# Kernel tuning notes

Measured on AMD Instinct MI355X. Metric: run time of the kernel, lower is better.

## Reference

```python
import jax, jax.numpy as jnp
import numpy as np

NUM_ELEMENTS = 100
EMBED_DIM = 256
HIDDEN_DIM = 512
NUM_HEADS = 8
NUM_MASKS = 1
NUM_GAUSSIANS = 50
RBF_RADIUS = 12.0
N_NODES = 20000
N_EDGES = 400000


def setup_inputs() -> dict:
    key = jax.random.key(0)
    ks = jax.random.split(key, 10)
    anum = jax.random.randint(ks[0], (N_NODES,), 0, NUM_ELEMENTS)
    edge_index = jax.random.randint(ks[1], (2, N_EDGES), 0, N_NODES)
    edge_to_src = jax.random.randint(ks[2], (N_EDGES,), 0, N_EDGES)
    dist = jax.random.uniform(ks[3], (N_EDGES,), jnp.float32) * RBF_RADIUS
    # learned parameters (init scales follow reset_parameters)
    emb_table = jax.random.normal(ks[4], (NUM_ELEMENTS ** 2, EMBED_DIM), jnp.float32)
    s_gate = np.sqrt(3.0 / 2.50663)
    gate_W = jax.random.uniform(ks[5], (HIDDEN_DIM, NUM_GAUSSIANS), jnp.float32, -s_gate, s_gate)
    in_dim = EMBED_DIM + NUM_GAUSSIANS
    s_emb = np.sqrt(3.0 / EMBED_DIM)
    W_emb = jax.random.uniform(ks[6], (HIDDEN_DIM, EMBED_DIM), jnp.float32, -s_emb, s_emb)
    W_rbf = jax.random.uniform(ks[7], (HIDDEN_DIM, NUM_GAUSSIANS), jnp.float32, -s_gate, s_gate)
    W_in = jnp.concatenate([W_emb, W_rbf], axis=1)  # [H, emb+G]
    b_in = jnp.zeros((HIDDEN_DIM,), jnp.float32)
    s_out = np.sqrt(1.0 / HIDDEN_DIM)
    W_out = jax.random.uniform(ks[8], (NUM_HEADS * NUM_MASKS, HIDDEN_DIM), jnp.float32, -s_out, s_out)
    b_out = jnp.zeros((NUM_HEADS * NUM_MASKS,), jnp.float32)
    return {"anum": anum, "edge_index": edge_index, "edge_to_src": edge_to_src,
            "dist": dist, "emb_table": emb_table, "gate_W": gate_W,
            "W_in": W_in, "b_in": b_in, "W_out": W_out, "b_out": b_out}


def _gaussian_smearing(dist):
    offset = jnp.linspace(0.0, RBF_RADIUS, NUM_GAUSSIANS, dtype=dist.dtype)
    coeff = -0.5 / (offset[1] - offset[0]) ** 2
    d = dist[:, None] - offset[None, :]  # [E, G]
    return jnp.exp(coeff * d * d)


def reference(anum, edge_index, edge_to_src, dist, emb_table, gate_W, W_in, b_in, W_out, b_out):
    rbf = _gaussian_smearing(dist)                                  # [E, G]
    pair_idx = anum[edge_index[0]] + NUM_ELEMENTS * anum[edge_index[1]]  # [E]
    emb = emb_table[pair_idx]                                       # [E, D]
    x = jnp.concatenate([emb[edge_to_src], rbf], axis=-1)           # [E, D+G]
    gate = rbf @ gate_W.T                                           # [E, H]
    h = jax.nn.silu(x @ W_in.T + b_in) * gate                       # gated ResMLP hidden
    att_bias = h @ W_out.T + b_out                                  # [E, heads*masks]
    att_bias = att_bias.reshape(dist.shape[0], NUM_HEADS, NUM_MASKS)
    return jnp.transpose(att_bias, (2, 1, 0))                       # [masks, heads, E]
```

## Files before the change

### kernel.cpp

```cpp
#include <hip/hip_runtime.h>
#include <hip/hip_bf16.h>

typedef unsigned short u16;
typedef unsigned int   uint;
typedef __attribute__((ext_vector_type(8))) short bf16x8;
typedef __attribute__((ext_vector_type(4))) float f32x4;

constexpr int NELEM = 100;
constexpr int EMBED = 256;
constexpr int HID   = 512;
constexpr int KX    = 306;
constexpr int G     = 50;
constexpr int M     = 64;
constexpr int THREADS = 512;

constexpr int WB_ELEMS = 32 * 10 * 64 * 8;
constexpr int GB_ELEMS = 32 * 2 * 64 * 8;
constexpr int OB_ELEMS = 16 * 64 * 8;
constexpr int WEIGHT_ELEMS = WB_ELEMS + GB_ELEMS + OB_ELEMS;
constexpr int NPREP = WEIGHT_ELEMS / THREADS;

__device__ __forceinline__ u16 f2bf(float x) {
    uint u = __float_as_uint(x);
    u = (u + 0x7fffu + ((u >> 16) & 1u)) >> 16;
    return (u16)u;
}
__device__ __forceinline__ uint pk2(float a, float b) {
    __hip_bfloat162 h = __float22bfloat162_rn(make_float2(a, b));
    return *reinterpret_cast<uint*>(&h);
}
__device__ __forceinline__ float bflo(uint u) { return __uint_as_float(u << 16); }
__device__ __forceinline__ float bfhi(uint u) { return __uint_as_float(u & 0xffff0000u); }
__device__ __forceinline__ float silu(float p) {
    return p * __builtin_amdgcn_rcpf(1.f + __expf(-p));
}
__device__ __forceinline__ f32x4 mfma16(bf16x8 a, bf16x8 b, f32x4 c) {
    return __builtin_amdgcn_mfma_f32_16x16x32_bf16(a, b, c, 0, 0, 0);
}

__global__ __launch_bounds__(THREADS)
void prep_hist_kernel(const float* __restrict__ W_in,
                      const float* __restrict__ gate_W,
                      const float* __restrict__ W_out,
                      const float* __restrict__ b_in,
                      const int* __restrict__ anum,
                      const int* __restrict__ edge_index,
                      const int* __restrict__ edge_to_src,
                      u16* __restrict__ Wb,
                      u16* __restrict__ Gb,
                      u16* __restrict__ Ob,
                      u16* __restrict__ pairids,
                      int* __restrict__ bins,
                      int E) {
    const int bid = blockIdx.x;
    const int t   = threadIdx.x;

    if (bid < NPREP) {
        int idx = bid * THREADS + t;
        if (idx < WB_ELEMS) {
            int j = idx & 7, lane = (idx >> 3) & 63, kn = idx >> 9;
            int ks = kn % 10, nt = kn / 10;
            int h = nt * 16 + (lane & 15);
            int k = ks * 32 + (lane >> 4) * 8 + j;
            float v = (k < KX) ? W_in[h * KX + k] : ((k == KX) ? b_in[h] : 0.f);
            Wb[idx] = f2bf(v);
        } else if (idx < WB_ELEMS + GB_ELEMS) {
            int i2 = idx - WB_ELEMS;
            int j = i2 & 7, lane = (i2 >> 3) & 63, kn = i2 >> 9;
            int ks = kn & 1, nt = kn >> 1;
            int h = nt * 16 + (lane & 15);
            int g = ks * 32 + (lane >> 4) * 8 + j;
            Gb[i2] = f2bf((g < G) ? gate_W[h * G + g] : 0.f);
        } else {
            int i2 = idx - WB_ELEMS - GB_ELEMS;
            int j = i2 & 7, lane = (i2 >> 3) & 63, s = i2 >> 9;
            int m = lane & 15, q = lane >> 4;
            int hid = s * 32 + (j >> 2) * 16 + q * 4 + (j & 3);
            Ob[i2] = f2bf((m < 8) ? W_out[m * HID + hid] : 0.f);
        }
        return;
    }
    int i = (bid - NPREP) * THREADS + t;
    if (i < E) {
        int src  = edge_to_src[i];
        int pair = anum[edge_index[src]] + NELEM * anum[edge_index[E + src]];
        pairids[i] = (u16)pair;
        atomicAdd(&bins[pair], 1);
    }
}

__global__ __launch_bounds__(THREADS)
void scan_kernel(int* __restrict__ bins, int npair) {
    __shared__ int lds[THREADS];
    const int t = threadIdx.x;
    const int chunk = (npair + THREADS - 1) / THREADS;
    const int lo = t * chunk;
    const int hi = min(lo + chunk, npair);
    int s = 0;
    for (int i = lo; i < hi; ++i) s += bins[i];
    lds[t] = s;
    __syncthreads();
    for (int off = 1; off < THREADS; off <<= 1) {
        int add = (t >= off) ? lds[t - off] : 0;
        __syncthreads();
        lds[t] += add;
        __syncthreads();
    }
    int excl = lds[t] - s;
    for (int i = lo; i < hi; ++i) {
        int c = bins[i];
        bins[i] = excl;
        excl += c;
    }
}

__global__ __launch_bounds__(THREADS)
void scatter_hpre_kernel(const float* __restrict__ table,
                         const u16* __restrict__ Wb,
                         const u16* __restrict__ pairids,
                         int* __restrict__ bins,
                         int* __restrict__ perm,
                         u16* __restrict__ spair,
                         float* __restrict__ hpreF,
                         u16*   __restrict__ hpreH,
                         int E, int npair, int nsc, int f32h) {
    __shared__ __align__(16) u16 af[8 * 4 * 64 * 8];
    const int bid = blockIdx.x;
    const int t   = threadIdx.x;

    if (bid < nsc) {
        int i = bid * THREADS + t;
        if (i < E) {
            int p   = pairids[i];
            int pos = atomicAdd(&bins[p], 1);
            perm[pos]  = i;
            spair[pos] = (u16)p;
        }
        return;
    }

    const int pb = bid - nsc;
    const int p0 = pb * M;
    const int wave = t >> 6, lane = t & 63;
    const int col = lane & 15, quad = lane >> 4;

    #pragma unroll
    for (int mt = 0; mt < 4; ++mt) {
        int p = p0 + mt * 16 + col;
        uint4 w = {0u, 0u, 0u, 0u};
        if (p < npair) {
            const float* s = table + (size_t)p * EMBED + wave * 32 + quad * 8;
            float4 v0 = ((const float4*)s)[0], v1 = ((const float4*)s)[1];
            w.x = pk2(v0.x, v0.y); w.y = pk2(v0.z, v0.w);
            w.z = pk2(v1.x, v1.y); w.w = pk2(v1.z, v1.w);
        }
        *(uint4*)&af[((wave * 4 + mt) * 64 + lane) * 8] = w;
    }
    __syncthreads();

    const f32x4 z4 = {0.f, 0.f, 0.f, 0.f};
    #pragma unroll
    for (int nh = 0; nh < 2; ++nh) {
        f32x4 acc[2][4];
        #pragma unroll
        for (int ntl = 0; ntl < 2; ++ntl)
            #pragma unroll
            for (int mt = 0; mt < 4; ++mt) acc[ntl][mt] = z4;
        #pragma unroll 2
        for (int ks = 0; ks < 8; ++ks) {
            bf16x8 a[4];
            #pragma unroll
            for (int mt = 0; mt < 4; ++mt)
                a[mt] = *(const bf16x8*)&af[((ks * 4 + mt) * 64 + lane) * 8];
            #pragma unroll
            for (int ntl = 0; ntl < 2; ++ntl) {
                int ntg = wave * 4 + nh * 2 + ntl;
                bf16x8 wf = *(const bf16x8*)&Wb[((ntg * 10 + ks) * 64 + lane) * 8];
                #pragma unroll
                for (int mt = 0; mt < 4; ++mt)
                    acc[ntl][mt] = mfma16(wf, a[mt], acc[ntl][mt]);
            }
        }
        #pragma unroll
        for (int ntl = 0; ntl < 2; ++ntl)
            #pragma unroll
            for (int mt = 0; mt < 4; ++mt) {
                int p = p0 + mt * 16 + col;
                if (p < npair) {
                    int hb = (wave * 4 + nh * 2 + ntl) * 16 + quad * 4;
                    if (f32h) {
                        *(f32x4*)(hpreF + (size_t)p * HID + hb) = acc[ntl][mt];
                    } else {
                        uint2 o;
                        o.x = pk2(acc[ntl][mt][0], acc[ntl][mt][1]);
                        o.y = pk2(acc[ntl][mt][2], acc[ntl][mt][3]);
                        *(uint2*)(hpreH + (size_t)p * HID + hb) = o;
                    }
                }
            }
    }
}

template <bool F32H>
__global__ __launch_bounds__(THREADS, 4)
void pair_embed_srt(const int* __restrict__ perm,
                    const u16* __restrict__ spair,
                    const float* __restrict__ dist,
                    const float* __restrict__ hpreF,
                    const u16*   __restrict__ hpreH,
                    const float* __restrict__ b_out,
                    const u16* __restrict__ Wb,
                    const u16* __restrict__ Gb,
                    const u16* __restrict__ Ob,
                    float* __restrict__ out,
                    int E) {
    __shared__ __align__(16) u16 smem[16384];
    __shared__ int   rowbase[M];
    __shared__ float dste[M];
    __shared__ int   oidx[M];
    u16*   afrag = smem;
    float* redf  = (float*)smem;

    const int t  = threadIdx.x;
    const int e0 = blockIdx.x * M;
    const int wave = t >> 6, lane = t & 63;
    const int col = lane & 15, quad = lane >> 4;

    if (t < M) {
        int slot = e0 + t;
        int pair = 0, orig = 0; float d = 0.f;
        if (slot < E) {
            orig = perm[slot];
            pair = spair[slot];
            d    = dist[orig];
        }
        rowbase[t] = pair * HID;
        dste[t]    = d;
        oidx[t]    = orig;
    }
    __syncthreads();

    int rbm[4];
    #pragma unroll
    for (int mt = 0; mt < 4; ++mt) rbm[mt] = rowbase[mt * 16 + col];

    f32x4 hp[2][4];
    uint2 hph[2][4];
    #pragma unroll
    for (int mt = 0; mt < 4; ++mt) {
        int base = rbm[mt] + (wave * 4) * 16 + quad * 4;
        if (F32H) {
            const float* p = hpreF + base;
            hp[0][mt] = *(const f32x4*)p;
            hp[1][mt] = *(const f32x4*)(p + 16);
        } else {
            const u16* p = hpreH + base;
            hph[0][mt] = *(const uint2*)p;
            hph[1][mt] = *(const uint2*)(p + 16);
        }
    }

    {
        const float sp    = 12.0f / 49.0f;
        const float coeff = -0.5f / (sp * sp);
        int ks = wave & 1, mtr = wave >> 1;
        float d  = dste[mtr * 16 + col];
        int   g0 = ks * 32 + quad * 8;
        float f[8];
        #pragma unroll
        for (int j = 0; j < 8; ++j) {
            int g = g0 + j;
            float dd = d - sp * (float)g;
            f[j] = (g < G) ? __expf(coeff * dd * dd) : ((g == G) ? 1.f : 0.f);
        }
        uint4 w;
        w.x = pk2(f[0], f[1]); w.y = pk2(f[2], f[3]);
        w.z = pk2(f[4], f[5]); w.w = pk2(f[6], f[7]);
        *(uint4*)&afrag[((ks * 4 + mtr) * 64 + lane) * 8] = w;
    }
    __syncthreads();

    const f32x4 z4 = {0.f, 0.f, 0.f, 0.f};
    f32x4 oacc[4] = {z4, z4, z4, z4};

    #pragma unroll
    for (int nh = 0; nh < 2; ++nh) {
        if (nh == 1) {
            #pragma unroll
            for (int mt = 0; mt < 4; ++mt) {
                int base = rbm[mt] + (wave * 4 + 2) * 16 + quad * 4;
                if (F32H) {
                    const float* p = hpreF + base;
                    hp[0][mt] = *(const f32x4*)p;
                    hp[1][mt] = *(const f32x4*)(p + 16);
                } else {
                    const u16* p = hpreH + base;
                    hph[0][mt] = *(const uint2*)p;
                    hph[1][mt] = *(const uint2*)(p + 16);
                }
            }
        }
        f32x4 acc[2][4], gacc[2][4];
        #pragma unroll
        for (int ntl = 0; ntl < 2; ++ntl)
            #pragma unroll
            for (int mt = 0; mt < 4; ++mt) {
                gacc[ntl][mt] = z4;
                if (F32H) {
                    acc[ntl][mt] = hp[ntl][mt];
                } else {
                    uint2 v = hph[ntl][mt];
                    f32x4 a = {bflo(v.x), bfhi(v.x), bflo(v.y), bfhi(v.y)};
                    acc[ntl][mt] = a;
                }
            }

        const u16* gb = &Gb[((wave * 4 + nh * 2) * 2 * 64 + lane) * 8];
        const u16* wb = &Wb[(((wave * 4 + nh * 2) * 10 + 8) * 64 + lane) * 8];
        #pragma unroll
        for (int ks = 0; ks < 2; ++ks) {
            bf16x8 a[4];
            #pragma unroll
            for (int mt = 0; mt < 4; ++mt)
                a[mt] = *(const bf16x8*)&afrag[((ks * 4 + mt) * 64 + lane) * 8];
            bf16x8 g0f = *(const bf16x8*)&gb[ks * 512];
            bf16x8 w0f = *(const bf16x8*)&wb[ks * 512];
            bf16x8 g1f = *(const bf16x8*)&gb[1024 + ks * 512];
            bf16x8 w1f = *(const bf16x8*)&wb[5120 + ks * 512];
            #pragma unroll
            for (int mt = 0; mt < 4; ++mt) gacc[0][mt] = mfma16(g0f, a[mt], gacc[0][mt]);
            #pragma unroll
            for (int mt = 0; mt < 4; ++mt) acc[0][mt]  = mfma16(w0f, a[mt], acc[0][mt]);
            #pragma unroll
            for (int mt = 0; mt < 4; ++mt) gacc[1][mt] = mfma16(g1f, a[mt], gacc[1][mt]);
            #pragma unroll
            for (int mt = 0; mt < 4; ++mt) acc[1][mt]  = mfma16(w1f, a[mt], acc[1][mt]);
        }

        bf16x8 obf = *(const bf16x8*)&Ob[(((wave << 1) | nh) * 64 + lane) * 8];
        #pragma unroll
        for (int mt = 0; mt < 4; ++mt) {
            uint4 hq;
            hq.x = pk2(silu(acc[0][mt][0]) * gacc[0][mt][0],
                       silu(acc[0][mt][1]) * gacc[0][mt][1]);
            hq.y = pk2(silu(acc[0][mt][2]) * gacc[0][mt][2],
                       silu(acc[0][mt][3]) * gacc[0][mt][3]);
            hq.z = pk2(silu(acc[1][mt][0]) * gacc[1][mt][0],
                       silu(acc[1][mt][1]) * gacc[1][mt][1]);
            hq.w = pk2(silu(acc[1][mt][2]) * gacc[1][mt][2],
                       silu(acc[1][mt][3]) * gacc[1][mt][3]);
            oacc[mt] = mfma16(obf, *(bf16x8*)&hq, oacc[mt]);
        }
    }
    __syncthreads();

    #pragma unroll
    for (int mt = 0; mt < 4; ++mt)
        *(f32x4*)&redf[((wave * 4 + mt) * 64 + lane) * 4] = oacc[mt];
    __syncthreads();

    {
        int head = t >> 6, el = t & 63;
        int mt = el >> 4, c = el & 15;
        int l  = (head >> 2) * 16 + c;
        int r  = head & 3;
        float s = 0.f;
        #pragma unroll
        for (int w = 0; w < 8; ++w)
            s += redf[((w * 4 + mt) * 64 + l) * 4 + r];
        int slot = e0 + el;
        if (slot < E) out[head * E + oidx[el]] = s + b_out[head];
    }
}

template <bool F32H>
__global__ __launch_bounds__(THREADS, 4)
void pair_embed_pre(const int* __restrict__ anum,
                    const int* __restrict__ edge_index,
                    const int* __restrict__ edge_to_src,
                    const float* __restrict__ dist,
                    const float* __restrict__ hpreF,
                    const u16*   __restrict__ hpreH,
                    const float* __restrict__ b_out,
                    const u16* __restrict__ Wb,
                    const u16* __restrict__ Gb,
                    const u16* __restrict__ Ob,
                    float* __restrict__ out,
                    int E) {
    __shared__ __align__(16) u16 smem[16384];
    __shared__ int   rowbase[M];
    __shared__ float dste[M];
    u16*   afrag = smem;
    float* redf  = (float*)smem;

    const int t  = threadIdx.x;
    const int e0 = blockIdx.x * M;
    const int wave = t >> 6, lane = t & 63;
    const int col = lane & 15, quad = lane >> 4;

    if (t < M) {
        int eg = e0 + t;
        int pair = 0; float d = 0.f;
        if (eg < E) {
            int src = edge_to_src[eg];
            pair = anum[edge_index[src]] + NELEM * anum[edge_index[E + src]];
            d = dist[eg];
        }
        rowbase[t] = pair * HID;
        dste[t]    = d;
    }
    __syncthreads();

    int rbm[4];
    #pragma unroll
    for (int mt = 0; mt < 4; ++mt) rbm[mt] = rowbase[mt * 16 + col];

    f32x4 hp[2][4];
    uint2 hph[2][4];
    #pragma unroll
    for (int mt = 0; mt < 4; ++mt) {
        int base = rbm[mt] + (wave * 4) * 16 + quad * 4;
        if (F32H) {
            const float* p = hpreF + base;
            hp[0][mt] = *(const f32x4*)p;
            hp[1][mt] = *(const f32x4*)(p + 16);
        } else {
            const u16* p = hpreH + base;
            hph[0][mt] = *(const uint2*)p;
            hph[1][mt] = *(const uint2*)(p + 16);
        }
    }

    {
        const float sp    = 12.0f / 49.0f;
        const float coeff = -0.5f / (sp * sp);
        int ks = wave & 1, mtr = wave >> 1;
        float d  = dste[mtr * 16 + col];
        int   g0 = ks * 32 + quad * 8;
        float f[8];
        #pragma unroll
        for (int j = 0; j < 8; ++j) {
            int g = g0 + j;
            float dd = d - sp * (float)g;
            f[j] = (g < G) ? __expf(coeff * dd * dd) : ((g == G) ? 1.f : 0.f);
        }
        uint4 w;
        w.x = pk2(f[0], f[1]); w.y = pk2(f[2], f[3]);
        w.z = pk2(f[4], f[5]); w.w = pk2(f[6], f[7]);
        *(uint4*)&afrag[((ks * 4 + mtr) * 64 + lane) * 8] = w;
    }
    __syncthreads();

    const f32x4 z4 = {0.f, 0.f, 0.f, 0.f};
    f32x4 oacc[4] = {z4, z4, z4, z4};

    #pragma unroll
    for (int nh = 0; nh < 2; ++nh) {
        if (nh == 1) {
            #pragma unroll
            for (int mt = 0; mt < 4; ++mt) {
                int base = rbm[mt] + (wave * 4 + 2) * 16 + quad * 4;
                if (F32H) {
                    const float* p = hpreF + base;
                    hp[0][mt] = *(const f32x4*)p;
                    hp[1][mt] = *(const f32x4*)(p + 16);
                } else {
                    const u16* p = hpreH + base;
                    hph[0][mt] = *(const uint2*)p;
                    hph[1][mt] = *(const uint2*)(p + 16);
                }
            }
        }
        f32x4 acc[2][4], gacc[2][4];
        #pragma unroll
        for (int ntl = 0; ntl < 2; ++ntl)
            #pragma unroll
            for (int mt = 0; mt < 4; ++mt) {
                gacc[ntl][mt] = z4;
                if (F32H) {
                    acc[ntl][mt] = hp[ntl][mt];
                } else {
                    uint2 v = hph[ntl][mt];
                    f32x4 a = {bflo(v.x), bfhi(v.x), bflo(v.y), bfhi(v.y)};
                    acc[ntl][mt] = a;
                }
            }

        const u16* gb = &Gb[((wave * 4 + nh * 2) * 2 * 64 + lane) * 8];
        const u16* wb = &Wb[(((wave * 4 + nh * 2) * 10 + 8) * 64 + lane) * 8];
        #pragma unroll
        for (int ks = 0; ks < 2; ++ks) {
            bf16x8 a[4];
            #pragma unroll
            for (int mt = 0; mt < 4; ++mt)
                a[mt] = *(const bf16x8*)&afrag[((ks * 4 + mt) * 64 + lane) * 8];
            bf16x8 g0f = *(const bf16x8*)&gb[ks * 512];
            bf16x8 w0f = *(const bf16x8*)&wb[ks * 512];
            bf16x8 g1f = *(const bf16x8*)&gb[1024 + ks * 512];
            bf16x8 w1f = *(const bf16x8*)&wb[5120 + ks * 512];
            #pragma unroll
            for (int mt = 0; mt < 4; ++mt) gacc[0][mt] = mfma16(g0f, a[mt], gacc[0][mt]);
            #pragma unroll
            for (int mt = 0; mt < 4; ++mt) acc[0][mt]  = mfma16(w0f, a[mt], acc[0][mt]);
            #pragma unroll
            for (int mt = 0; mt < 4; ++mt) gacc[1][mt] = mfma16(g1f, a[mt], gacc[1][mt]);
            #pragma unroll
            for (int mt = 0; mt < 4; ++mt) acc[1][mt]  = mfma16(w1f, a[mt], acc[1][mt]);
        }

        bf16x8 obf = *(const bf16x8*)&Ob[(((wave << 1) | nh) * 64 + lane) * 8];
        #pragma unroll
        for (int mt = 0; mt < 4; ++mt) {
            uint4 hq;
            hq.x = pk2(silu(acc[0][mt][0]) * gacc[0][mt][0],
                       silu(acc[0][mt][1]) * gacc[0][mt][1]);
            hq.y = pk2(silu(acc[0][mt][2]) * gacc[0][mt][2],
                       silu(acc[0][mt][3]) * gacc[0][mt][3]);
            hq.z = pk2(silu(acc[1][mt][0]) * gacc[1][mt][0],
                       silu(acc[1][mt][1]) * gacc[1][mt][1]);
            hq.w = pk2(silu(acc[1][mt][2]) * gacc[1][mt][2],
                       silu(acc[1][mt][3]) * gacc[1][mt][3]);
            oacc[mt] = mfma16(obf, *(bf16x8*)&hq, oacc[mt]);
        }
    }
    __syncthreads();

    #pragma unroll
    for (int mt = 0; mt < 4; ++mt)
        *(f32x4*)&redf[((wave * 4 + mt) * 64 + lane) * 4] = oacc[mt];
    __syncthreads();

    {
        int head = t >> 6, el = t & 63;
        int mt = el >> 4, c = el & 15;
        int l  = (head >> 2) * 16 + c;
        int r  = head & 3;
        float s = 0.f;
        #pragma unroll
        for (int w = 0; w < 8; ++w)
            s += redf[((w * 4 + mt) * 64 + l) * 4 + r];
        int eg = e0 + el;
        if (eg < E) out[head * E + eg] = s + b_out[head];
    }
}

extern "C" void kernel_launch(void* const* d_in, const int* in_sizes, int n_in,
                              void* d_out, int out_size, void* d_ws, size_t ws_size,
                              hipStream_t stream) {
    const int*   anum        = (const int*)d_in[0];
    const int*   edge_index  = (const int*)d_in[1];
    const int*   edge_to_src = (const int*)d_in[2];
    const float* dist        = (const float*)d_in[3];
    const float* emb_table   = (const float*)d_in[4];
    const float* gate_W      = (const float*)d_in[5];
    const float* W_in        = (const float*)d_in[6];
    const float* b_in        = (const float*)d_in[7];
    const float* W_out       = (const float*)d_in[8];
    const float* b_out       = (const float*)d_in[9];
    const int E     = in_sizes[3];
    const int TBL   = in_sizes[4];
    const int NPAIR = TBL / EMBED;

    u16* Wb = (u16*)d_ws;
    u16* Gb = Wb + WB_ELEMS;
    u16* Ob = Gb + GB_ELEMS;
    const size_t WSW  = (size_t)WEIGHT_ELEMS * 2;
    const size_t hb32 = (size_t)NPAIR * HID * 4;
    const size_t hb16 = (size_t)NPAIR * HID * 2;
    const size_t sortx = (size_t)E * 8 + (size_t)NPAIR * 4;

    int mode;
    if      (ws_size >= WSW + hb32 + sortx) mode = 4;
    else if (ws_size >= WSW + hb16 + sortx) mode = 3;
    else if (ws_size >= WSW + hb32)         mode = 2;
    else                                    mode = 1;

    const size_t hb = (mode == 4 || mode == 2) ? hb32 : hb16;
    char*  hbase   = (char*)d_ws + WSW;
    float* hpreF   = (float*)hbase;
    u16*   hpreH   = (u16*)hbase;
    char*  q       = hbase + hb;
    int*   perm    = (int*)q;
    u16*   pairids = (u16*)(q + (size_t)E * 4);
    u16*   spair   = (u16*)(q + (size_t)E * 6);
    int*   bins    = (int*)(q + (size_t)E * 8);

    const int nhist   = (E + THREADS - 1) / THREADS;
    const int npb     = (NPAIR + M - 1) / M;
    const int nblocks = (E + M - 1) / M;
    const int f32h    = (mode == 4 || mode == 2) ? 1 : 0;

    if (mode >= 3) {
        hipMemsetAsync(bins, 0, (size_t)NPAIR * 4, stream);
        prep_hist_kernel<<<NPREP + nhist, THREADS, 0, stream>>>(
            W_in, gate_W, W_out, b_in, anum, edge_index, edge_to_src,
            Wb, Gb, Ob, pairids, bins, E);
        scan_kernel<<<1, THREADS, 0, stream>>>(bins, NPAIR);
        scatter_hpre_kernel<<<nhist + npb, THREADS, 0, stream>>>(
            emb_table, Wb, pairids, bins, perm, spair, hpreF, hpreH,
            E, NPAIR, nhist, f32h);
        if (mode == 4) {
            pair_embed_srt<true><<<nblocks, THREADS, 0, stream>>>(
                perm, spair, dist, hpreF, hpreH, b_out, Wb, Gb, Ob, (float*)d_out, E);
        } else {
            pair_embed_srt<false><<<nblocks, THREADS, 0, stream>>>(
                perm, spair, dist, hpreF, hpreH, b_out, Wb, Gb, Ob, (float*)d_out, E);
        }
    } else {
        prep_hist_kernel<<<NPREP, THREADS, 0, stream>>>(
            W_in, gate_W, W_out, b_in, anum, edge_index, edge_to_src,
            Wb, Gb, Ob, pairids, bins, E);
        scatter_hpre_kernel<<<npb, THREADS, 0, stream>>>(
            emb_table, Wb, pairids, bins, perm, spair, hpreF, hpreH,
            E, NPAIR, 0, f32h);
        if (mode == 2) {
            pair_embed_pre<true><<<nblocks, THREADS, 0, stream>>>(
                anum, edge_index, edge_to_src, dist, hpreF, hpreH,
                b_out, Wb, Gb, Ob, (float*)d_out, E);
        } else {
            pair_embed_pre<false><<<nblocks, THREADS, 0, stream>>>(
                anum, edge_index, edge_to_src, dist, hpreF, hpreH,
                b_out, Wb, Gb, Ob, (float*)d_out, E);
        }
    }
}
```

Baseline: 293.2 us.

## Restructure sort pipeline: fuse hist with hpre GEMM, pack sorted edges, drop bf16 modes

```diff
diff --git a/kernel.cpp b/kernel.cpp
--- a/kernel.cpp
+++ b/kernel.cpp
@@ -18,7 +18,6 @@
 constexpr int GB_ELEMS = 32 * 2 * 64 * 8;
 constexpr int OB_ELEMS = 16 * 64 * 8;
 constexpr int WEIGHT_ELEMS = WB_ELEMS + GB_ELEMS + OB_ELEMS;
-constexpr int NPREP = WEIGHT_ELEMS / THREADS;
 
 __device__ __forceinline__ u16 f2bf(float x) {
     uint u = __float_as_uint(x);
@@ -29,8 +28,6 @@
     __hip_bfloat162 h = __float22bfloat162_rn(make_float2(a, b));
     return *reinterpret_cast<uint*>(&h);
 }
-__device__ __forceinline__ float bflo(uint u) { return __uint_as_float(u << 16); }
-__device__ __forceinline__ float bfhi(uint u) { return __uint_as_float(u & 0xffff0000u); }
 __device__ __forceinline__ float silu(float p) {
     return p * __builtin_amdgcn_rcpf(1.f + __expf(-p));
 }
@@ -39,24 +36,20 @@
 }
 
 __global__ __launch_bounds__(THREADS)
-void prep_hist_kernel(const float* __restrict__ W_in,
-                      const float* __restrict__ gate_W,
-                      const float* __restrict__ W_out,
-                      const float* __restrict__ b_in,
-                      const int* __restrict__ anum,
-                      const int* __restrict__ edge_index,
-                      const int* __restrict__ edge_to_src,
-                      u16* __restrict__ Wb,
-                      u16* __restrict__ Gb,
-                      u16* __restrict__ Ob,
-                      u16* __restrict__ pairids,
-                      int* __restrict__ bins,
-                      int E) {
-    const int bid = blockIdx.x;
-    const int t   = threadIdx.x;
-
-    if (bid < NPREP) {
-        int idx = bid * THREADS + t;
+void init_kernel(const float* __restrict__ W_in,
+                 const float* __restrict__ gate_W,
+                 const float* __restrict__ W_out,
+                 const float* __restrict__ b_in,
+                 u16* __restrict__ Wb,
+                 u16* __restrict__ Gb,
+                 u16* __restrict__ Ob,
+                 int* __restrict__ bins,
+                 int npair, int do_sort) {
+    const int gtid = blockIdx.x * THREADS + threadIdx.x;
+    const int gsz  = gridDim.x * THREADS;
+    if (do_sort)
+        for (int i = gtid; i < npair; i += gsz) bins[i] = 0;
+    for (int idx = gtid; idx < WEIGHT_ELEMS; idx += gsz) {
         if (idx < WB_ELEMS) {
             int j = idx & 7, lane = (idx >> 3) & 63, kn = idx >> 9;
             int ks = kn % 10, nt = kn / 10;
@@ -78,14 +71,96 @@
             int hid = s * 32 + (j >> 2) * 16 + q * 4 + (j & 3);
             Ob[i2] = f2bf((m < 8) ? W_out[m * HID + hid] : 0.f);
         }
+    }
+}
+
+__global__ __launch_bounds__(THREADS)
+void hist_hpre_kernel(const int* __restrict__ anum,
+                      const int* __restrict__ edge_index,
+                      const int* __restrict__ edge_to_src,
+                      const float* __restrict__ table,
+                      const u16* __restrict__ Wb,
+                      u16* __restrict__ pairids,
+                      int* __restrict__ bins,
+                      float* __restrict__ hpreF,
+                      int E, int npair, int nh4) {
+    __shared__ __align__(16) u16 af[8 * 4 * 64 * 8];
+    const int bid = blockIdx.x;
+    const int t   = threadIdx.x;
+
+    if (bid < nh4) {
+        const int base = bid * (THREADS * 4) + t;
+        int idxv[4], srcv[4], n0[4], n1[4];
+        #pragma unroll
+        for (int k = 0; k < 4; ++k) idxv[k] = base + k * THREADS;
+        #pragma unroll
+        for (int k = 0; k < 4; ++k)
+            if (idxv[k] < E) srcv[k] = edge_to_src[idxv[k]];
+        #pragma unroll
+        for (int k = 0; k < 4; ++k)
+            if (idxv[k] < E) { n0[k] = edge_index[srcv[k]]; n1[k] = edge_index[E + srcv[k]]; }
+        #pragma unroll
+        for (int k = 0; k < 4; ++k)
+            if (idxv[k] < E) {
+                int pair = anum[n0[k]] + NELEM * anum[n1[k]];
+                pairids[idxv[k]] = (u16)pair;
+                atomicAdd(&bins[pair], 1);
+            }
         return;
     }
-    int i = (bid - NPREP) * THREADS + t;
-    if (i < E) {
-        int src  = edge_to_src[i];
-        int pair = anum[edge_index[src]] + NELEM * anum[edge_index[E + src]];
-        pairids[i] = (u16)pair;
-        atomicAdd(&bins[pair], 1);
+
+    const int pb = bid - nh4;
+    const int p0 = pb * M;
+    const int wave = t >> 6, lane = t & 63;
+    const int col = lane & 15, quad = lane >> 4;
+
+    #pragma unroll
+    for (int mt = 0; mt < 4; ++mt) {
+        int p = p0 + mt * 16 + col;
+        uint4 w = {0u, 0u, 0u, 0u};
+        if (p < npair) {
+            const float* s = table + (size_t)p * EMBED + wave * 32 + quad * 8;
+            float4 v0 = ((const float4*)s)[0], v1 = ((const float4*)s)[1];
+            w.x = pk2(v0.x, v0.y); w.y = pk2(v0.z, v0.w);
+            w.z = pk2(v1.x, v1.y); w.w = pk2(v1.z, v1.w);
+        }
+        *(uint4*)&af[((wave * 4 + mt) * 64 + lane) * 8] = w;
+    }
+    __syncthreads();
+
+    const f32x4 z4 = {0.f, 0.f, 0.f, 0.f};
+    #pragma unroll
+    for (int nh = 0; nh < 2; ++nh) {
+        f32x4 acc[2][4];
+        #pragma unroll
+        for (int ntl = 0; ntl < 2; ++ntl)
+            #pragma unroll
+            for (int mt = 0; mt < 4; ++mt) acc[ntl][mt] = z4;
+        #pragma unroll 2
+        for (int ks = 0; ks < 8; ++ks) {
+            bf16x8 a[4];
+            #pragma unroll
+            for (int mt = 0; mt < 4; ++mt)
+                a[mt] = *(const bf16x8*)&af[((ks * 4 + mt) * 64 + lane) * 8];
+            #pragma unroll
+            for (int ntl = 0; ntl < 2; ++ntl) {
+                int ntg = wave * 4 + nh * 2 + ntl;
+                bf16x8 wf = *(const bf16x8*)&Wb[((ntg * 10 + ks) * 64 + lane) * 8];
+                #pragma unroll
+                for (int mt = 0; mt < 4; ++mt)
+                    acc[ntl][mt] = mfma16(wf, a[mt], acc[ntl][mt]);
+            }
+        }
+        #pragma unroll
+        for (int ntl = 0; ntl < 2; ++ntl)
+            #pragma unroll
+            for (int mt = 0; mt < 4; ++mt) {
+                int p = p0 + mt * 16 + col;
+                if (p < npair) {
+                    int hb = (wave * 4 + nh * 2 + ntl) * 16 + quad * 4;
+                    *(f32x4*)(hpreF + (size_t)p * HID + hb) = acc[ntl][mt];
+                }
+            }
     }
 }
 
@@ -115,99 +190,29 @@
 }
 
 __global__ __launch_bounds__(THREADS)
-void scatter_hpre_kernel(const float* __restrict__ table,
-                         const u16* __restrict__ Wb,
-                         const u16* __restrict__ pairids,
-                         int* __restrict__ bins,
-                         int* __restrict__ perm,
-                         u16* __restrict__ spair,
-                         float* __restrict__ hpreF,
-                         u16*   __restrict__ hpreH,
-                         int E, int npair, int nsc, int f32h) {
-    __shared__ __align__(16) u16 af[8 * 4 * 64 * 8];
-    const int bid = blockIdx.x;
-    const int t   = threadIdx.x;
-
-    if (bid < nsc) {
-        int i = bid * THREADS + t;
-        if (i < E) {
-            int p   = pairids[i];
-            int pos = atomicAdd(&bins[p], 1);
-            perm[pos]  = i;
-            spair[pos] = (u16)p;
-        }
-        return;
-    }
-
-    const int pb = bid - nsc;
-    const int p0 = pb * M;
-    const int wave = t >> 6, lane = t & 63;
-    const int col = lane & 15, quad = lane >> 4;
-
-    #pragma unroll
-    for (int mt = 0; mt < 4; ++mt) {
-        int p = p0 + mt * 16 + col;
-        uint4 w = {0u, 0u, 0u, 0u};
-        if (p < npair) {
-            const float* s = table + (size_t)p * EMBED + wave * 32 + quad * 8;
-            float4 v0 = ((const float4*)s)[0], v1 = ((const float4*)s)[1];
-            w.x = pk2(v0.x, v0.y); w.y = pk2(v0.z, v0.w);
-            w.z = pk2(v1.x, v1.y); w.w = pk2(v1.z, v1.w);
-        }
-        *(uint4*)&af[((wave * 4 + mt) * 64 + lane) * 8] = w;
-    }
-    __syncthreads();
-
-    const f32x4 z4 = {0.f, 0.f, 0.f, 0.f};
-    #pragma unroll
-    for (int nh = 0; nh < 2; ++nh) {
-        f32x4 acc[2][4];
-        #pragma unroll
-        for (int ntl = 0; ntl < 2; ++ntl)
-            #pragma unroll
-            for (int mt = 0; mt < 4; ++mt) acc[ntl][mt] = z4;
-        #pragma unroll 2
-        for (int ks = 0; ks < 8; ++ks) {
-            bf16x8 a[4];
-            #pragma unroll
-            for (int mt = 0; mt < 4; ++mt)
-                a[mt] = *(const bf16x8*)&af[((ks * 4 + mt) * 64 + lane) * 8];
-            #pragma unroll
-            for (int ntl = 0; ntl < 2; ++ntl) {
-                int ntg = wave * 4 + nh * 2 + ntl;
-                bf16x8 wf = *(const bf16x8*)&Wb[((ntg * 10 + ks) * 64 + lane) * 8];
-                #pragma unroll
-                for (int mt = 0; mt < 4; ++mt)
-                    acc[ntl][mt] = mfma16(wf, a[mt], acc[ntl][mt]);
-            }
-        }
-        #pragma unroll
-        for (int ntl = 0; ntl < 2; ++ntl)
-            #pragma unroll
-            for (int mt = 0; mt < 4; ++mt) {
-                int p = p0 + mt * 16 + col;
-                if (p < npair) {
-                    int hb = (wave * 4 + nh * 2 + ntl) * 16 + quad * 4;
-                    if (f32h) {
-                        *(f32x4*)(hpreF + (size_t)p * HID + hb) = acc[ntl][mt];
-                    } else {
-                        uint2 o;
-                        o.x = pk2(acc[ntl][mt][0], acc[ntl][mt][1]);
-                        o.y = pk2(acc[ntl][mt][2], acc[ntl][mt][3]);
-                        *(uint2*)(hpreH + (size_t)p * HID + hb) = o;
-                    }
-                }
-            }
-    }
-}
-
-template <bool F32H>
-__global__ __launch_bounds__(THREADS, 4)
-void pair_embed_srt(const int* __restrict__ perm,
-                    const u16* __restrict__ spair,
+void scatter_kernel(const u16* __restrict__ pairids,
+                    int* __restrict__ bins,
+                    uint2* __restrict__ sedge,
+                    int E) {
+    const int base = blockIdx.x * (THREADS * 4) + threadIdx.x;
+    int idxv[4], pv[4];
+    #pragma unroll
+    for (int k = 0; k < 4; ++k) idxv[k] = base + k * THREADS;
+    #pragma unroll
+    for (int k = 0; k < 4; ++k)
+        if (idxv[k] < E) pv[k] = pairids[idxv[k]];
+    #pragma unroll
+    for (int k = 0; k < 4; ++k)
+        if (idxv[k] < E) {
+            int pos = atomicAdd(&bins[pv[k]], 1);
+            sedge[pos] = make_uint2((uint)idxv[k], (uint)pv[k]);
+        }
+}
+
+__global__ __launch_bounds__(THREADS, 3)
+void pair_embed_srt(const uint2* __restrict__ sedge,
                     const float* __restrict__ dist,
                     const float* __restrict__ hpreF,
-                    const u16*   __restrict__ hpreH,
                     const float* __restrict__ b_out,
                     const u16* __restrict__ Wb,
                     const u16* __restrict__ Gb,
@@ -228,15 +233,12 @@
 
     if (t < M) {
         int slot = e0 + t;
-        int pair = 0, orig = 0; float d = 0.f;
-        if (slot < E) {
-            orig = perm[slot];
-            pair = spair[slot];
-            d    = dist[orig];
-        }
-        rowbase[t] = pair * HID;
+        uint2 se = make_uint2(0u, 0u);
+        float d = 0.f;
+        if (slot < E) { se = sedge[slot]; d = dist[se.x]; }
+        rowbase[t] = (int)se.y * HID;
         dste[t]    = d;
-        oidx[t]    = orig;
+        oidx[t]    = (int)se.x;
     }
     __syncthreads();
 
@@ -244,20 +246,12 @@
     #pragma unroll
     for (int mt = 0; mt < 4; ++mt) rbm[mt] = rowbase[mt * 16 + col];
 
-    f32x4 hp[2][4];
-    uint2 hph[2][4];
+    f32x4 hp0[2][4];
     #pragma unroll
     for (int mt = 0; mt < 4; ++mt) {
-        int base = rbm[mt] + (wave * 4) * 16 + quad * 4;
-        if (F32H) {
-            const float* p = hpreF + base;
-            hp[0][mt] = *(const f32x4*)p;
-            hp[1][mt] = *(const f32x4*)(p + 16);
-        } else {
-            const u16* p = hpreH + base;
-            hph[0][mt] = *(const uint2*)p;
-            hph[1][mt] = *(const uint2*)(p + 16);
-        }
+        const float* p = hpreF + rbm[mt] + wave * 64 + quad * 4;
+        hp0[0][mt] = *(const f32x4*)p;
+        hp0[1][mt] = *(const f32x4*)(p + 16);
     }
 
     {
@@ -280,39 +274,26 @@
     }
     __syncthreads();
 
+    f32x4 hp1[2][4];
+    #pragma unroll
+    for (int mt = 0; mt < 4; ++mt) {
+        const float* p = hpreF + rbm[mt] + wave * 64 + 32 + quad * 4;
+        hp1[0][mt] = *(const f32x4*)p;
+        hp1[1][mt] = *(const f32x4*)(p + 16);
+    }
+
     const f32x4 z4 = {0.f, 0.f, 0.f, 0.f};
     f32x4 oacc[4] = {z4, z4, z4, z4};
 
     #pragma unroll
     for (int nh = 0; nh < 2; ++nh) {
-        if (nh == 1) {
-            #pragma unroll
-            for (int mt = 0; mt < 4; ++mt) {
-                int base = rbm[mt] + (wave * 4 + 2) * 16 + quad * 4;
-                if (F32H) {
-                    const float* p = hpreF + base;
-                    hp[0][mt] = *(const f32x4*)p;
-                    hp[1][mt] = *(const f32x4*)(p + 16);
-                } else {
-                    const u16* p = hpreH + base;
-                    hph[0][mt] = *(const uint2*)p;
-                    hph[1][mt] = *(const uint2*)(p + 16);
-                }
-            }
-        }
         f32x4 acc[2][4], gacc[2][4];
         #pragma unroll
         for (int ntl = 0; ntl < 2; ++ntl)
             #pragma unroll
             for (int mt = 0; mt < 4; ++mt) {
                 gacc[ntl][mt] = z4;
-                if (F32H) {
-                    acc[ntl][mt] = hp[ntl][mt];
-                } else {
-                    uint2 v = hph[ntl][mt];
-                    f32x4 a = {bflo(v.x), bfhi(v.x), bflo(v.y), bfhi(v.y)};
-                    acc[ntl][mt] = a;
-                }
+                acc[ntl][mt]  = nh ? hp1[ntl][mt] : hp0[ntl][mt];
             }
 
         const u16* gb = &Gb[((wave * 4 + nh * 2) * 2 * 64 + lane) * 8];
@@ -373,20 +354,18 @@
     }
 }
 
-template <bool F32H>
 __global__ __launch_bounds__(THREADS, 4)
-void pair_embed_pre(const int* __restrict__ anum,
-                    const int* __restrict__ edge_index,
-                    const int* __restrict__ edge_to_src,
-                    const float* __restrict__ dist,
-                    const float* __restrict__ hpreF,
-                    const u16*   __restrict__ hpreH,
-                    const float* __restrict__ b_out,
-                    const u16* __restrict__ Wb,
-                    const u16* __restrict__ Gb,
-                    const u16* __restrict__ Ob,
-                    float* __restrict__ out,
-                    int E) {
+void pair_embed_unsrt(const int* __restrict__ anum,
+                      const int* __restrict__ edge_index,
+                      const int* __restrict__ edge_to_src,
+                      const float* __restrict__ dist,
+                      const float* __restrict__ hpreF,
+                      const float* __restrict__ b_out,
+                      const u16* __restrict__ Wb,
+                      const u16* __restrict__ Gb,
+                      const u16* __restrict__ Ob,
+                      float* __restrict__ out,
+                      int E) {
     __shared__ __align__(16) u16 smem[16384];
     __shared__ int   rowbase[M];
     __shared__ float dste[M];
@@ -416,19 +395,11 @@
     for (int mt = 0; mt < 4; ++mt) rbm[mt] = rowbase[mt * 16 + col];
 
     f32x4 hp[2][4];
-    uint2 hph[2][4];
     #pragma unroll
     for (int mt = 0; mt < 4; ++mt) {
-        int base = rbm[mt] + (wave * 4) * 16 + quad * 4;
-        if (F32H) {
-            const float* p = hpreF + base;
-            hp[0][mt] = *(const f32x4*)p;
-            hp[1][mt] = *(const f32x4*)(p + 16);
-        } else {
-            const u16* p = hpreH + base;
-            hph[0][mt] = *(const uint2*)p;
-            hph[1][mt] = *(const uint2*)(p + 16);
-        }
+        const float* p = hpreF + rbm[mt] + wave * 64 + quad * 4;
+        hp[0][mt] = *(const f32x4*)p;
+        hp[1][mt] = *(const f32x4*)(p + 16);
     }
 
     {
@@ -459,16 +430,9 @@
         if (nh == 1) {
             #pragma unroll
             for (int mt = 0; mt < 4; ++mt) {
-                int base = rbm[mt] + (wave * 4 + 2) * 16 + quad * 4;
-                if (F32H) {
-                    const float* p = hpreF + base;
-                    hp[0][mt] = *(const f32x4*)p;
-                    hp[1][mt] = *(const f32x4*)(p + 16);
-                } else {
-                    const u16* p = hpreH + base;
-                    hph[0][mt] = *(const uint2*)p;
-                    hph[1][mt] = *(const uint2*)(p + 16);
-                }
+                const float* p = hpreF + rbm[mt] + wave * 64 + 32 + quad * 4;
+                hp[0][mt] = *(const f32x4*)p;
+                hp[1][mt] = *(const f32x4*)(p + 16);
             }
         }
         f32x4 acc[2][4], gacc[2][4];
@@ -477,13 +441,7 @@
             #pragma unroll
             for (int mt = 0; mt < 4; ++mt) {
                 gacc[ntl][mt] = z4;
-                if (F32H) {
-                    acc[ntl][mt] = hp[ntl][mt];
-                } else {
-                    uint2 v = hph[ntl][mt];
-                    f32x4 a = {bflo(v.x), bfhi(v.x), bflo(v.y), bfhi(v.y)};
-                    acc[ntl][mt] = a;
-                }
+                acc[ntl][mt]  = hp[ntl][mt];
             }
 
         const u16* gb = &Gb[((wave * 4 + nh * 2) * 2 * 64 + lane) * 8];
@@ -565,62 +523,44 @@
     u16* Gb = Wb + WB_ELEMS;
     u16* Ob = Gb + GB_ELEMS;
     const size_t WSW  = (size_t)WEIGHT_ELEMS * 2;
-    const size_t hb32 = (size_t)NPAIR * HID * 4;
-    const size_t hb16 = (size_t)NPAIR * HID * 2;
-    const size_t sortx = (size_t)E * 8 + (size_t)NPAIR * 4;
-
-    int mode;
-    if      (ws_size >= WSW + hb32 + sortx) mode = 4;
-    else if (ws_size >= WSW + hb16 + sortx) mode = 3;
-    else if (ws_size >= WSW + hb32)         mode = 2;
-    else                                    mode = 1;
-
-    const size_t hb = (mode == 4 || mode == 2) ? hb32 : hb16;
+    const size_t HB   = (size_t)NPAIR * HID * 4;
+    const size_t SEB  = (size_t)E * 8;
+    const size_t PIB  = ((size_t)E * 2 + 15) & ~(size_t)15;
+    const size_t BINB = (size_t)NPAIR * 4;
+
+    const size_t szSorted = WSW + HB + SEB + PIB + BINB;
+    const size_t szUnsrt  = WSW + HB;
+    const int mode = (ws_size >= szSorted) ? 1 : ((ws_size >= szUnsrt) ? 0 : -1);
+    if (mode < 0) return;
+
     char*  hbase   = (char*)d_ws + WSW;
     float* hpreF   = (float*)hbase;
-    u16*   hpreH   = (u16*)hbase;
-    char*  q       = hbase + hb;
-    int*   perm    = (int*)q;
-    u16*   pairids = (u16*)(q + (size_t)E * 4);
-    u16*   spair   = (u16*)(q + (size_t)E * 6);
-    int*   bins    = (int*)(q + (size_t)E * 8);
-
-    const int nhist   = (E + THREADS - 1) / THREADS;
-    const int npb     = (NPAIR + M - 1) / M;
+    uint2* sedge   = (uint2*)(hbase + HB);
+    u16*   pairids = (u16*)(hbase + HB + SEB);
+    int*   bins    = (int*)(hbase + HB + SEB + PIB);
+
+    const int NH4     = (E + THREADS * 4 - 1) / (THREADS * 4);
+    const int NPB     = (NPAIR + M - 1) / M;
     const int nblocks = (E + M - 1) / M;
-    const int f32h    = (mode == 4 || mode == 2) ? 1 : 0;
-
-    if (mode >= 3) {
-        hipMemsetAsync(bins, 0, (size_t)NPAIR * 4, stream);
-        prep_hist_kernel<<<NPREP + nhist, THREADS, 0, stream>>>(
-            W_in, gate_W, W_out, b_in, anum, edge_index, edge_to_src,
-            Wb, Gb, Ob, pairids, bins, E);
+
+    if (mode == 1) {
+        init_kernel<<<256, THREADS, 0, stream>>>(
+            W_in, gate_W, W_out, b_in, Wb, Gb, Ob, bins, NPAIR, 1);
+        hist_hpre_kernel<<<NH4 + NPB, THREADS, 0, stream>>>(
+            anum, edge_index, edge_to_src, emb_table, Wb,
+            pairids, bins, hpreF, E, NPAIR, NH4);
         scan_kernel<<<1, THREADS, 0, stream>>>(bins, NPAIR);
-        scatter_hpre_kernel<<<nhist + npb, THREADS, 0, stream>>>(
-            emb_table, Wb, pairids, bins, perm, spair, hpreF, hpreH,
-            E, NPAIR, nhist, f32h);
-        if (mode == 4) {
-            pair_embed_srt<true><<<nblocks, THREADS, 0, stream>>>(
-                perm, spair, dist, hpreF, hpreH, b_out, Wb, Gb, Ob, (float*)d_out, E);
-        } else {
-            pair_embed_srt<false><<<nblocks, THREADS, 0, stream>>>(
-                perm, spair, dist, hpreF, hpreH, b_out, Wb, Gb, Ob, (float*)d_out, E);
-        }
+        scatter_kernel<<<NH4, THREADS, 0, stream>>>(pairids, bins, sedge, E);
+        pair_embed_srt<<<nblocks, THREADS, 0, stream>>>(
+            sedge, dist, hpreF, b_out, Wb, Gb, Ob, (float*)d_out, E);
     } else {
-        prep_hist_kernel<<<NPREP, THREADS, 0, stream>>>(
-            W_in, gate_W, W_out, b_in, anum, edge_index, edge_to_src,
-            Wb, Gb, Ob, pairids, bins, E);
-        scatter_hpre_kernel<<<npb, THREADS, 0, stream>>>(
-            emb_table, Wb, pairids, bins, perm, spair, hpreF, hpreH,
-            E, NPAIR, 0, f32h);
-        if (mode == 2) {
-            pair_embed_pre<true><<<nblocks, THREADS, 0, stream>>>(
-                anum, edge_index, edge_to_src, dist, hpreF, hpreH,
-                b_out, Wb, Gb, Ob, (float*)d_out, E);
-        } else {
-            pair_embed_pre<false><<<nblocks, THREADS, 0, stream>>>(
-                anum, edge_index, edge_to_src, dist, hpreF, hpreH,
-                b_out, Wb, Gb, Ob, (float*)d_out, E);
-        }
-    }
-}
+        init_kernel<<<256, THREADS, 0, stream>>>(
+            W_in, gate_W, W_out, b_in, Wb, Gb, Ob, bins, NPAIR, 0);
+        hist_hpre_kernel<<<NPB, THREADS, 0, stream>>>(
+            anum, edge_index, edge_to_src, emb_table, Wb,
+            pairids, bins, hpreF, E, NPAIR, 0);
+        pair_embed_unsrt<<<nblocks, THREADS, 0, stream>>>(
+            anum, edge_index, edge_to_src, dist, hpreF, b_out,
+            Wb, Gb, Ob, (float*)d_out, E);
+    }
+}
```

Result: slower. 340.3 us (+16.1%).
